# Kernel optimization log

Measured on AMD Instinct MI355X. Metric: run time of the kernel, lower is better.

The kernel has to match this reference:

```python
import jax, jax.numpy as jnp
import numpy as np
import math

Ds = 2048
N = 16384
M = 1024


def setup_inputs() -> dict:
    key = jax.random.key(0)
    kD, kS, kW = jax.random.split(key, 3)
    D = jax.random.normal(kD, (N, Ds), dtype=jnp.float32)
    S = jax.random.normal(kS, (M, Ds), dtype=jnp.float32)
    W = jax.random.normal(kW, (Ds, Ds), dtype=jnp.float32) * 0.01  # init.normal std=0.01
    return {"D": D, "S": S, "W": W}


def reference(D, S, W):
    ds = D.shape[1]
    temperature = 1.0
    # cross-attention: [n, m]
    scores = (D @ S.T) / (math.sqrt(ds) * temperature)
    att_weight = jax.nn.softmax(scores, axis=1)
    att_S = att_weight @ S  # [n, Ds]
    # bilinear per row: logits[i] = D[i] . (W @ att_S[i])  -> fused einsum
    logits = jnp.einsum('nd,de,ne->n', D, W, att_S)
    log_prob = jnp.sum(jax.nn.log_sigmoid(logits))
    return log_prob
```

## Files before the change

### kernel.cpp

```cpp
#include <hip/hip_runtime.h>
#include <stdint.h>

typedef unsigned short u16;
typedef unsigned int u32;
typedef __attribute__((ext_vector_type(8))) short bf16x8;
typedef __attribute__((ext_vector_type(4))) float f32x4;
typedef __attribute__((ext_vector_type(4))) u32 u32x4;

#define DS 2048
#define NROWS 16384
#define MS 1024
#define K2 2048

__device__ __forceinline__ u16 f2bf(float f) {
  u32 u = __float_as_uint(f);
  u32 r = (u + 0x7fffu + ((u >> 16) & 1u)) >> 16;
  return (u16)r;
}

__device__ __forceinline__ void gload16(const u16* g, u16* l) {
  __builtin_amdgcn_global_load_lds(
      (const __attribute__((address_space(1))) void*)g,
      (__attribute__((address_space(3))) void*)l, 16, 0, 0);
}

#define DSR(d, a, IMM) \
  asm volatile("ds_read_b128 %0, %1 offset:%c2" : "=v"(d) : "v"(a), "n"(IMM))
#define CVTPK(d, lo, hi) \
  asm("v_cvt_pk_bf16_f32 %0, %1, %2" : "=v"(d) : "v"(lo), "v"(hi))
#define LGKM(N)                                              \
  asm volatile("s_waitcnt lgkmcnt(" #N ")" ::: "memory");    \
  __builtin_amdgcn_sched_barrier(0)
#define VMW(N) asm volatile("s_waitcnt vmcnt(" #N ")" ::: "memory")
#define SB0() __builtin_amdgcn_sched_barrier(0)
#define PRIO1() __builtin_amdgcn_s_setprio(1)
#define PRIO0() __builtin_amdgcn_s_setprio(0)
#define BAR() __builtin_amdgcn_s_barrier()

#define CVT8(dst, lo, hi)                                         \
  do {                                                            \
    u32 _c0, _c1, _c2, _c3;                                       \
    CVTPK(_c0, lo[0], lo[1]); CVTPK(_c1, lo[2], lo[3]);           \
    CVTPK(_c2, hi[0], hi[1]); CVTPK(_c3, hi[2], hi[3]);           \
    u32x4 _q = {_c0, _c1, _c2, _c3};                              \
    dst = *(bf16x8*)&_q;                                          \
  } while (0)

__global__ __launch_bounds__(256) void k_pre(const float* __restrict__ D,
                                             const float* __restrict__ S,
                                             const float* __restrict__ W,
                                             u16* __restrict__ Dbf,
                                             u16* __restrict__ Bt) {
  __shared__ float lsA[2][64 * 32];
  __shared__ float lsB[2][128 * 32];
  const int bid = blockIdx.x;
  const int tid = threadIdx.x;

  if (bid >= 256) {
    if (bid < 2304) {
      size_t i = (size_t)(bid - 256) * 256 + tid;
#pragma unroll
      for (int it = 0; it < 16; ++it, i += (size_t)2048 * 256) {
        float4 v = ((const float4*)D)[i];
        ushort4 o;
        o.x = f2bf(v.x); o.y = f2bf(v.y); o.z = f2bf(v.z); o.w = f2bf(v.w);
        ((ushort4*)Dbf)[i] = o;
      }
    } else {
      size_t j = (size_t)(bid - 2304) * 256 + tid;
#pragma unroll
      for (int it = 0; it < 16; ++it, j += (size_t)128 * 256) {
        float4 v = ((const float4*)S)[j];
        ushort4 o;
        o.x = f2bf(v.x); o.y = f2bf(v.y); o.z = f2bf(v.z); o.w = f2bf(v.w);
        int m = (int)(j >> 9), c4 = (int)(j & 511);
        ((ushort4*)Bt)[(size_t)m * 1024 + c4] = o;
      }
    }
    return;
  }

  const int wid = tid >> 6, lane = tid & 63;
  const int brow = (bid >> 4) * 64;
  const int bcol = (bid & 15) * 128;
  const int wm = wid >> 1, wn = wid & 1;
  const int l15 = lane & 15, s0 = lane >> 4;

  const int sr = tid >> 3;
  const int soct = (tid & 7) ^ (sr & 7);
  const float* gS = S + (size_t)(brow + sr) * 2048 + soct * 4;
  const float* gW = W + (size_t)(bcol + sr) * 2048 + soct * 4;

  const u32 lbA = (u32)(uintptr_t)&lsA[0][0];
  const u32 lbB = (u32)(uintptr_t)&lsB[0][0];
  const u32 swz = (u32)(((2 * s0) ^ (l15 & 7)) * 16);
  const u32 aA = lbA + (u32)(wm * 32 + l15) * 128 + swz;
  const u32 aAx = aA ^ 16u;
  const u32 aB = lbB + (u32)(wn * 64 + l15) * 128 + swz;
  const u32 aBx = aB ^ 16u;

  f32x4 acc[2][4];
#pragma unroll
  for (int i = 0; i < 2; ++i)
#pragma unroll
    for (int j = 0; j < 4; ++j) acc[i][j] = (f32x4){0.f, 0.f, 0.f, 0.f};

#define VSTG(b, kt)                                                              \
  do {                                                                           \
    gload16((const u16*)(gS + (kt)),             (u16*)(&lsA[b][0] + wid * 256)); \
    gload16((const u16*)(gS + 32 * 2048 + (kt)), (u16*)(&lsA[b][1024] + wid * 256)); \
    gload16((const u16*)(gW + (kt)),             (u16*)(&lsB[b][0] + wid * 256)); \
    gload16((const u16*)(gW + 32 * 2048 + (kt)), (u16*)(&lsB[b][1024] + wid * 256)); \
    gload16((const u16*)(gW + 64 * 2048 + (kt)), (u16*)(&lsB[b][2048] + wid * 256)); \
    gload16((const u16*)(gW + 96 * 2048 + (kt)), (u16*)(&lsB[b][3072] + wid * 256)); \
  } while (0)

  VSTG(0, 0);
#pragma unroll 1
  for (int t = 0; t < 64; ++t) {
    const int b = t & 1;
    const u32 oA = (u32)(b * 8192), oB = (u32)(b * 16384);
    if (t < 63) {
      VSTG(b ^ 1, (t + 1) * 32);
      VMW(6);
    } else {
      VMW(0);
    }
    BAR(); SB0();
    f32x4 qa0, qa1, qa2, qa3;
    f32x4 qb0, qb1, qb2, qb3, qb4, qb5, qb6, qb7;
    DSR(qa0, aA + oA, 0);     DSR(qa1, aAx + oA, 0);
    DSR(qa2, aA + oA, 2048);  DSR(qa3, aAx + oA, 2048);
    DSR(qb0, aB + oB, 0);     DSR(qb1, aBx + oB, 0);
    DSR(qb2, aB + oB, 2048);  DSR(qb3, aBx + oB, 2048);
    DSR(qb4, aB + oB, 4096);  DSR(qb5, aBx + oB, 4096);
    DSR(qb6, aB + oB, 6144);  DSR(qb7, aBx + oB, 6144);
    LGKM(0);
    bf16x8 af[2], bfr[4];
    CVT8(af[0], qa0, qa1); CVT8(af[1], qa2, qa3);
    CVT8(bfr[0], qb0, qb1); CVT8(bfr[1], qb2, qb3);
    CVT8(bfr[2], qb4, qb5); CVT8(bfr[3], qb6, qb7);
    PRIO1();
#pragma unroll
    for (int mi = 0; mi < 2; ++mi)
#pragma unroll
      for (int ni = 0; ni < 4; ++ni)
        acc[mi][ni] = __builtin_amdgcn_mfma_f32_16x16x32_bf16(af[mi], bfr[ni],
                                                              acc[mi][ni], 0, 0, 0);
    PRIO0(); SB0();
    BAR();
  }
#undef VSTG

  const int crow0 = brow + wm * 32 + s0 * 4;
  const int ccol0 = bcol + wn * 64 + l15;
  u16* C = Bt + 2048;
#pragma unroll
  for (int mi = 0; mi < 2; ++mi)
#pragma unroll
    for (int ni = 0; ni < 4; ++ni)
#pragma unroll
      for (int r = 0; r < 4; ++r)
        C[(size_t)(crow0 + mi * 16 + r) * 4096 + (ccol0 + ni * 16)] =
            f2bf(acc[mi][ni][r]);
}

#define SINV 0.022097086912079608f

#define RD_A0(k0, k1, dst)                              \
  DSR(dst[0][0], k0, 0);     DSR(dst[0][1], k1, 0);     \
  DSR(dst[1][0], k0, 2048);  DSR(dst[1][1], k1, 2048);  \
  DSR(dst[2][0], k0, 4096);  DSR(dst[2][1], k1, 4096);  \
  DSR(dst[3][0], k0, 6144);  DSR(dst[3][1], k1, 6144)
#define RD_A1(k0, k1, dst)                              \
  DSR(dst[0][0], k0, 16384); DSR(dst[0][1], k1, 16384); \
  DSR(dst[1][0], k0, 18432); DSR(dst[1][1], k1, 18432); \
  DSR(dst[2][0], k0, 20480); DSR(dst[2][1], k1, 20480); \
  DSR(dst[3][0], k0, 22528); DSR(dst[3][1], k1, 22528)
#define RD_B0(k0, k1, dst)                              \
  DSR(dst[0][0], k0, 0);     DSR(dst[0][1], k1, 0);     \
  DSR(dst[1][0], k0, 2048);  DSR(dst[1][1], k1, 2048)
#define RD_B1(k0, k1, dst)                              \
  DSR(dst[0][0], k0, 16384); DSR(dst[0][1], k1, 16384); \
  DSR(dst[1][0], k0, 18432); DSR(dst[1][1], k1, 18432)

#define MMAQ(AF, BQ, QM, QN)                                                       \
  do {                                                                             \
    _Pragma("unroll") for (int mi = 0; mi < 4; ++mi)                               \
        _Pragma("unroll") for (int ni = 0; ni < 2; ++ni) {                         \
      acc[QM][QN][mi][ni] = __builtin_amdgcn_mfma_f32_16x16x32_bf16(               \
          AF[mi][0], BQ[ni][0], acc[QM][QN][mi][ni], 0, 0, 0);                     \
      acc[QM][QN][mi][ni] = __builtin_amdgcn_mfma_f32_16x16x32_bf16(               \
          AF[mi][1], BQ[ni][1], acc[QM][QN][mi][ni], 0, 0, 0);                     \
    }                                                                              \
  } while (0)

#define STGA(b, h, kt)                                                            \
  do {                                                                            \
    gload16(pA + (size_t)((h) * 128) * K2 + (kt),                                 \
            &lds[(b) * 32768 + (h) * 8192 + wid * 512]);                          \
    gload16(pA + (size_t)((h) * 128 + 64) * K2 + (kt),                            \
            &lds[(b) * 32768 + (h) * 8192 + 4096 + wid * 512]);                   \
  } while (0)
#define STGB(b, h, kt)                                                            \
  do {                                                                            \
    gload16(pB + (size_t)((h) * 128) * K2 + (kt),                                 \
            &lds[(b) * 32768 + 16384 + (h) * 8192 + wid * 512]);                  \
    gload16(pB + (size_t)((h) * 128 + 64) * K2 + (kt),                            \
            &lds[(b) * 32768 + 16384 + (h) * 8192 + 4096 + wid * 512]);           \
  } while (0)

__global__ __launch_bounds__(512, 2) void k_gemm8(const u16* __restrict__ A,
                                                  const u16* __restrict__ Bt,
                                                  float* __restrict__ Pnd) {
  extern __shared__ u16 lds[];
  const int tid = threadIdx.x;
  const int wid = tid >> 6;
  const int lane = tid & 63;
  const int bid = blockIdx.x;
  const int swz = (bid & 7) * 64 + (bid >> 3);
  const int by = swz >> 3, bx = swz & 7;
  const int brow = by * 256, bcol = bx * 256;
  const int wm = wid >> 2, wn = wid & 3;
  const int l15 = lane & 15, s0 = lane >> 4;

  const int tr = tid >> 3;
  const int scol = ((tid & 7) ^ (tr & 7)) << 3;
  const u16* pA = A + (size_t)(brow + tr) * K2 + scol;
  const u16* pB = Bt + (size_t)(bcol + tr) * K2 + scol;

  const u32 lb = (u32)(uintptr_t)(&lds[0]);
  const u32 xorp = ((u32)(s0 ^ (lane & 7))) << 4;
  const u32 aA00 = lb + ((u32)(wm * 64 + l15) << 7) + xorp;
  const u32 aA01 = aA00 ^ 64u;
  const u32 aA10 = aA00 + 65536u;
  const u32 aA11 = aA10 ^ 64u;
  const u32 aB00 = lb + 32768u + ((u32)(wn * 32 + l15) << 7) + xorp;
  const u32 aB01 = aB00 ^ 64u;
  const u32 aB10 = aB00 + 65536u;
  const u32 aB11 = aB10 ^ 64u;

  f32x4 acc[2][2][4][2];
#pragma unroll
  for (int a = 0; a < 2; ++a)
#pragma unroll
    for (int b = 0; b < 2; ++b)
#pragma unroll
      for (int c = 0; c < 4; ++c)
#pragma unroll
        for (int d = 0; d < 2; ++d) acc[a][b][c][d] = (f32x4){0.f, 0.f, 0.f, 0.f};

  bf16x8 afA[4][2], afB[4][2], bq0[2][2], bq1[2][2];

  STGA(0, 0, 0); STGB(0, 0, 0); STGB(0, 1, 0); STGA(0, 1, 0);
  STGA(1, 0, 64);
  VMW(2);
  BAR();
  RD_A0(aA00, aA01, afA);
  RD_B0(aB00, aB01, bq0);

  int kb = 0;
#pragma unroll 1
  for (int j = 0; j < 15; ++j, kb += 128) {
    STGB(1, 0, kb + 64);
    RD_B1(aB00, aB01, bq1);
    LGKM(4); PRIO1(); MMAQ(afA, bq0, 0, 0); PRIO0();
    STGB(1, 1, kb + 64);
    STGA(1, 1, kb + 64);
    RD_A1(aA00, aA01, afB);
    LGKM(8); PRIO1(); MMAQ(afA, bq1, 0, 1); PRIO0(); VMW(4); BAR();
    LGKM(0); PRIO1(); MMAQ(afB, bq0, 1, 0); PRIO0();
    STGA(0, 0, kb + 128);
    STGB(0, 0, kb + 128);
    RD_A0(aA10, aA11, afA);
    RD_B0(aB10, aB11, bq0);
    LGKM(12); PRIO1(); MMAQ(afB, bq1, 1, 1); PRIO0(); VMW(4); BAR();
    STGB(0, 1, kb + 128);
    RD_B1(aB10, aB11, bq1);
    LGKM(4); PRIO1(); MMAQ(afA, bq0, 0, 0); PRIO0();
    STGA(0, 1, kb + 128);
    RD_A1(aA10, aA11, afB);
    LGKM(8); PRIO1(); MMAQ(afA, bq1, 0, 1); PRIO0(); VMW(4); BAR();
    LGKM(0); PRIO1(); MMAQ(afB, bq0, 1, 0); PRIO0();
    STGA(1, 0, kb + 192);
    RD_A0(aA00, aA01, afA);
    RD_B0(aB00, aB01, bq0);
    LGKM(12); PRIO1(); MMAQ(afB, bq1, 1, 1); PRIO0(); VMW(2); BAR();
  }
  {
    STGB(1, 0, kb + 64);
    RD_B1(aB00, aB01, bq1);
    LGKM(4); PRIO1(); MMAQ(afA, bq0, 0, 0); PRIO0();
    STGB(1, 1, kb + 64);
    STGA(1, 1, kb + 64);
    RD_A1(aA00, aA01, afB);
    LGKM(8); PRIO1(); MMAQ(afA, bq1, 0, 1); PRIO0(); VMW(4); BAR();
    LGKM(0); PRIO1(); MMAQ(afB, bq0, 1, 0); PRIO0();
    RD_A0(aA10, aA11, afA);
    RD_B0(aB10, aB11, bq0);
    LGKM(12); PRIO1(); MMAQ(afB, bq1, 1, 1); PRIO0(); VMW(0); BAR();
    RD_B1(aB10, aB11, bq1);
    LGKM(4); PRIO1(); MMAQ(afA, bq0, 0, 0); PRIO0();
    RD_A1(aA10, aA11, afB);
    LGKM(8); PRIO1(); MMAQ(afA, bq1, 0, 1); PRIO0();
    LGKM(0); PRIO1(); MMAQ(afB, bq0, 1, 0); MMAQ(afB, bq1, 1, 1); PRIO0();
  }

  __syncthreads();
  float* red = (float*)&lds[0];

#pragma unroll
  for (int qm = 0; qm < 2; ++qm)
#pragma unroll
    for (int mi = 0; mi < 4; ++mi)
#pragma unroll
      for (int r = 0; r < 4; ++r) {
        float num = 0.f, den = 0.f;
#pragma unroll
        for (int qn = 0; qn < 2; ++qn)
#pragma unroll
          for (int ni = 0; ni < 2; ++ni) {
            float v = acc[qm][qn][mi][ni][r];
            float g = __shfl_xor(v, 1);
            float e = __expf(v * SINV);
            num += e * g;
            den += e;
          }
        num += __shfl_xor(num, 2); den += __shfl_xor(den, 2);
        num += __shfl_xor(num, 4); den += __shfl_xor(den, 4);
        num += __shfl_xor(num, 8); den += __shfl_xor(den, 8);
        if (l15 == 0) {
          int slot = qm * 16 + mi * 4 + r;
          red[((wid * 32 + slot) * 4 + s0) * 2 + 0] = num;
          red[((wid * 32 + slot) * 4 + s0) * 2 + 1] = den;
        }
      }
  __syncthreads();
  {
    int rloc = tid >> 1, which = tid & 1;
    int qm = rloc >> 7, wmr = (rloc >> 6) & 1, mi = (rloc >> 4) & 3;
    int lg = (rloc >> 2) & 3, r = rloc & 3;
    int slot = qm * 16 + mi * 4 + r;
    float v = 0.f;
#pragma unroll
    for (int w2 = 0; w2 < 4; ++w2)
      v += red[(((wmr * 4 + w2) * 32 + slot) * 4 + lg) * 2 + which];
    Pnd[((size_t)(brow + rloc) * 8 + bx) * 2 + which] = v;
  }
}

__global__ __launch_bounds__(256) void k_rowfinal(const float* __restrict__ Pnd,
                                                  float* __restrict__ part) {
  int row = blockIdx.x * 256 + threadIdx.x;
  const float4* p = (const float4*)(Pnd + (size_t)row * 16);
  float num = 0.f, den = 0.f;
#pragma unroll
  for (int i = 0; i < 4; ++i) {
    float4 v = p[i];
    num += v.x + v.z;
    den += v.y + v.w;
  }
  float logit = num / den;
  float ls = (logit >= 0.f) ? -log1pf(__expf(-logit))
                            : (logit - log1pf(__expf(logit)));
  __shared__ float red[4];
#pragma unroll
  for (int off = 32; off > 0; off >>= 1) ls += __shfl_down(ls, off);
  if ((threadIdx.x & 63) == 0) red[threadIdx.x >> 6] = ls;
  __syncthreads();
  if (threadIdx.x == 0) part[blockIdx.x] = red[0] + red[1] + red[2] + red[3];
}

__global__ __launch_bounds__(64) void k_final64(const float* __restrict__ part,
                                                float* __restrict__ out) {
  float v = part[threadIdx.x];
#pragma unroll
  for (int off = 32; off > 0; off >>= 1) v += __shfl_down(v, off);
  if (threadIdx.x == 0) out[0] = v;
}

extern "C" void kernel_launch(void* const* d_in, const int* in_sizes, int n_in,
                              void* d_out, int out_size, void* d_ws, size_t ws_size,
                              hipStream_t stream) {
  const float* D = (const float*)d_in[0];
  const float* S = (const float*)d_in[1];
  const float* W = (const float*)d_in[2];

  char* w = (char*)d_ws;
  u16* Dbf = (u16*)w; w += (size_t)NROWS * DS * 2;
  u16* Bt = (u16*)w;  w += (size_t)DS * DS * 2;
  float* Pnd = (float*)w; w += (size_t)NROWS * 16 * 4;
  float* part = (float*)w;

  (void)hipFuncSetAttribute((const void*)k_gemm8,
                            hipFuncAttributeMaxDynamicSharedMemorySize, 131072);

  k_pre<<<2432, 256, 0, stream>>>(D, S, W, Dbf, Bt);
  k_gemm8<<<512, 512, 131072, stream>>>(Dbf, Bt, Pnd);
  k_rowfinal<<<NROWS / 256, 256, 0, stream>>>(Pnd, part);
  k_final64<<<1, 64, 0, stream>>>(part, (float*)d_out);
}
```

Baseline: 167.1 us.

## Split-K the S·W precompute across two thread groups and reorder main GEMM LDS reads

The prologue kernel now runs 512 threads per block. In the GEMM blocks, two 256-thread groups each handle half of the K dimension with separate LDS buffers, and their partial accumulators are reduced through shared memory before the bf16 store. The conversion blocks process half as many iterations per thread. Separately, the main GEMM loop issues its LDS fragment reads earlier, before the corresponding MFMAs, with adjusted lgkmcnt waits, to hide LDS latency better. The cost is more LDS use and an extra reduction and barrier in the prologue, which lowers occupancy.

```diff
diff --git a/kernel.cpp b/kernel.cpp
--- a/kernel.cpp
+++ b/kernel.cpp
@@ -46,30 +46,29 @@
     dst = *(bf16x8*)&_q;                                          \
   } while (0)
 
-__global__ __launch_bounds__(256) void k_pre(const float* __restrict__ D,
+__global__ __launch_bounds__(512) void k_pre(const float* __restrict__ D,
                                              const float* __restrict__ S,
                                              const float* __restrict__ W,
                                              u16* __restrict__ Dbf,
                                              u16* __restrict__ Bt) {
-  __shared__ float lsA[2][64 * 32];
-  __shared__ float lsB[2][128 * 32];
+  extern __shared__ float ldsf[];
   const int bid = blockIdx.x;
   const int tid = threadIdx.x;
 
   if (bid >= 256) {
     if (bid < 2304) {
-      size_t i = (size_t)(bid - 256) * 256 + tid;
-#pragma unroll
-      for (int it = 0; it < 16; ++it, i += (size_t)2048 * 256) {
+      size_t i = (size_t)(bid - 256) * 512 + tid;
+#pragma unroll
+      for (int it = 0; it < 8; ++it, i += (size_t)2048 * 512) {
         float4 v = ((const float4*)D)[i];
         ushort4 o;
         o.x = f2bf(v.x); o.y = f2bf(v.y); o.z = f2bf(v.z); o.w = f2bf(v.w);
         ((ushort4*)Dbf)[i] = o;
       }
     } else {
-      size_t j = (size_t)(bid - 2304) * 256 + tid;
-#pragma unroll
-      for (int it = 0; it < 16; ++it, j += (size_t)128 * 256) {
+      size_t j = (size_t)(bid - 2304) * 512 + tid;
+#pragma unroll
+      for (int it = 0; it < 8; ++it, j += (size_t)128 * 512) {
         float4 v = ((const float4*)S)[j];
         ushort4 o;
         o.x = f2bf(v.x); o.y = f2bf(v.y); o.z = f2bf(v.z); o.w = f2bf(v.w);
@@ -80,23 +79,26 @@
     return;
   }
 
-  const int wid = tid >> 6, lane = tid & 63;
+  const int g = tid >> 8;
+  const int gtid = tid & 255;
+  const int wid = gtid >> 6, lane = tid & 63;
   const int brow = (bid >> 4) * 64;
   const int bcol = (bid & 15) * 128;
   const int wm = wid >> 1, wn = wid & 1;
   const int l15 = lane & 15, s0 = lane >> 4;
 
-  const int sr = tid >> 3;
-  const int soct = (tid & 7) ^ (sr & 7);
-  const float* gS = S + (size_t)(brow + sr) * 2048 + soct * 4;
-  const float* gW = W + (size_t)(bcol + sr) * 2048 + soct * 4;
-
-  const u32 lbA = (u32)(uintptr_t)&lsA[0][0];
-  const u32 lbB = (u32)(uintptr_t)&lsB[0][0];
+  const int sr = gtid >> 3;
+  const int soct = (gtid & 7) ^ (sr & 7);
+  const float* gS = S + (size_t)(brow + sr) * 2048 + g * 1024 + soct * 4;
+  const float* gW = W + (size_t)(bcol + sr) * 2048 + g * 1024 + soct * 4;
+
+  float* myA = ldsf + g * 12288;
+  float* myB = myA + 4096;
+  const u32 lbg = (u32)(uintptr_t)myA;
   const u32 swz = (u32)(((2 * s0) ^ (l15 & 7)) * 16);
-  const u32 aA = lbA + (u32)(wm * 32 + l15) * 128 + swz;
+  const u32 aA = lbg + (u32)(wm * 32 + l15) * 128 + swz;
   const u32 aAx = aA ^ 16u;
-  const u32 aB = lbB + (u32)(wn * 64 + l15) * 128 + swz;
+  const u32 aB = lbg + 16384u + (u32)(wn * 64 + l15) * 128 + swz;
   const u32 aBx = aB ^ 16u;
 
   f32x4 acc[2][4];
@@ -105,22 +107,22 @@
 #pragma unroll
     for (int j = 0; j < 4; ++j) acc[i][j] = (f32x4){0.f, 0.f, 0.f, 0.f};
 
-#define VSTG(b, kt)                                                              \
-  do {                                                                           \
-    gload16((const u16*)(gS + (kt)),             (u16*)(&lsA[b][0] + wid * 256)); \
-    gload16((const u16*)(gS + 32 * 2048 + (kt)), (u16*)(&lsA[b][1024] + wid * 256)); \
-    gload16((const u16*)(gW + (kt)),             (u16*)(&lsB[b][0] + wid * 256)); \
-    gload16((const u16*)(gW + 32 * 2048 + (kt)), (u16*)(&lsB[b][1024] + wid * 256)); \
-    gload16((const u16*)(gW + 64 * 2048 + (kt)), (u16*)(&lsB[b][2048] + wid * 256)); \
-    gload16((const u16*)(gW + 96 * 2048 + (kt)), (u16*)(&lsB[b][3072] + wid * 256)); \
+#define VSTG(b, kt)                                                               \
+  do {                                                                            \
+    gload16((const u16*)(gS + (kt)),             (u16*)(myA + (b)*2048 + wid*256)); \
+    gload16((const u16*)(gS + 32 * 2048 + (kt)), (u16*)(myA + (b)*2048 + 1024 + wid*256)); \
+    gload16((const u16*)(gW + (kt)),             (u16*)(myB + (b)*4096 + wid*256)); \
+    gload16((const u16*)(gW + 32 * 2048 + (kt)), (u16*)(myB + (b)*4096 + 1024 + wid*256)); \
+    gload16((const u16*)(gW + 64 * 2048 + (kt)), (u16*)(myB + (b)*4096 + 2048 + wid*256)); \
+    gload16((const u16*)(gW + 96 * 2048 + (kt)), (u16*)(myB + (b)*4096 + 3072 + wid*256)); \
   } while (0)
 
   VSTG(0, 0);
 #pragma unroll 1
-  for (int t = 0; t < 64; ++t) {
+  for (int t = 0; t < 32; ++t) {
     const int b = t & 1;
     const u32 oA = (u32)(b * 8192), oB = (u32)(b * 16384);
-    if (t < 63) {
+    if (t < 31) {
       VSTG(b ^ 1, (t + 1) * 32);
       VMW(6);
     } else {
@@ -152,17 +154,31 @@
   }
 #undef VSTG
 
-  const int crow0 = brow + wm * 32 + s0 * 4;
-  const int ccol0 = bcol + wn * 64 + l15;
-  u16* C = Bt + 2048;
-#pragma unroll
-  for (int mi = 0; mi < 2; ++mi)
-#pragma unroll
-    for (int ni = 0; ni < 4; ++ni)
-#pragma unroll
-      for (int r = 0; r < 4; ++r)
-        C[(size_t)(crow0 + mi * 16 + r) * 4096 + (ccol0 + ni * 16)] =
-            f2bf(acc[mi][ni][r]);
+  __syncthreads();
+  float* part = ldsf;
+  if (g == 1) {
+#pragma unroll
+    for (int mi = 0; mi < 2; ++mi)
+#pragma unroll
+      for (int ni = 0; ni < 4; ++ni)
+        *(f32x4*)&part[gtid * 36 + mi * 16 + ni * 4] = acc[mi][ni];
+  }
+  __syncthreads();
+  if (g == 0) {
+    const int crow0 = brow + wm * 32 + s0 * 4;
+    const int ccol0 = bcol + wn * 64 + l15;
+    u16* C = Bt + 2048;
+#pragma unroll
+    for (int mi = 0; mi < 2; ++mi)
+#pragma unroll
+      for (int ni = 0; ni < 4; ++ni) {
+        f32x4 p = *(const f32x4*)&part[gtid * 36 + mi * 16 + ni * 4];
+#pragma unroll
+        for (int r = 0; r < 4; ++r)
+          C[(size_t)(crow0 + mi * 16 + r) * 4096 + (ccol0 + ni * 16)] =
+              f2bf(acc[mi][ni][r] + p[r]);
+      }
+  }
 }
 
 #define SINV 0.022097086912079608f
@@ -262,46 +278,52 @@
   int kb = 0;
 #pragma unroll 1
   for (int j = 0; j < 15; ++j, kb += 128) {
+    RD_B1(aB00, aB01, bq1);
+    RD_A1(aA00, aA01, afB);
+    LGKM(12); PRIO1(); MMAQ(afA, bq0, 0, 0); PRIO0();
     STGB(1, 0, kb + 64);
-    RD_B1(aB00, aB01, bq1);
-    LGKM(4); PRIO1(); MMAQ(afA, bq0, 0, 0); PRIO0();
+    LGKM(8); PRIO1(); MMAQ(afA, bq1, 0, 1); PRIO0();
     STGB(1, 1, kb + 64);
     STGA(1, 1, kb + 64);
-    RD_A1(aA00, aA01, afB);
-    LGKM(8); PRIO1(); MMAQ(afA, bq1, 0, 1); PRIO0(); VMW(4); BAR();
-    LGKM(0); PRIO1(); MMAQ(afB, bq0, 1, 0); PRIO0();
+    VMW(4); BAR();
+    RD_A0(aA10, aA11, afA);
+    LGKM(8); PRIO1(); MMAQ(afB, bq0, 1, 0); PRIO0();
+    RD_B0(aB10, aB11, bq0);
     STGA(0, 0, kb + 128);
     STGB(0, 0, kb + 128);
-    RD_A0(aA10, aA11, afA);
-    RD_B0(aB10, aB11, bq0);
-    LGKM(12); PRIO1(); MMAQ(afB, bq1, 1, 1); PRIO0(); VMW(4); BAR();
+    LGKM(12); PRIO1(); MMAQ(afB, bq1, 1, 1); PRIO0();
+    VMW(4); BAR();
+    RD_B1(aB10, aB11, bq1);
+    RD_A1(aA10, aA11, afB);
+    LGKM(12); PRIO1(); MMAQ(afA, bq0, 0, 0); PRIO0();
     STGB(0, 1, kb + 128);
-    RD_B1(aB10, aB11, bq1);
-    LGKM(4); PRIO1(); MMAQ(afA, bq0, 0, 0); PRIO0();
+    LGKM(8); PRIO1(); MMAQ(afA, bq1, 0, 1); PRIO0();
     STGA(0, 1, kb + 128);
-    RD_A1(aA10, aA11, afB);
-    LGKM(8); PRIO1(); MMAQ(afA, bq1, 0, 1); PRIO0(); VMW(4); BAR();
-    LGKM(0); PRIO1(); MMAQ(afB, bq0, 1, 0); PRIO0();
+    VMW(4); BAR();
+    RD_A0(aA00, aA01, afA);
+    LGKM(8); PRIO1(); MMAQ(afB, bq0, 1, 0); PRIO0();
+    RD_B0(aB00, aB01, bq0);
     STGA(1, 0, kb + 192);
-    RD_A0(aA00, aA01, afA);
-    RD_B0(aB00, aB01, bq0);
-    LGKM(12); PRIO1(); MMAQ(afB, bq1, 1, 1); PRIO0(); VMW(2); BAR();
+    LGKM(12); PRIO1(); MMAQ(afB, bq1, 1, 1); PRIO0();
+    VMW(2); BAR();
   }
   {
+    RD_B1(aB00, aB01, bq1);
+    RD_A1(aA00, aA01, afB);
+    LGKM(12); PRIO1(); MMAQ(afA, bq0, 0, 0); PRIO0();
     STGB(1, 0, kb + 64);
-    RD_B1(aB00, aB01, bq1);
-    LGKM(4); PRIO1(); MMAQ(afA, bq0, 0, 0); PRIO0();
+    LGKM(8); PRIO1(); MMAQ(afA, bq1, 0, 1); PRIO0();
     STGB(1, 1, kb + 64);
     STGA(1, 1, kb + 64);
-    RD_A1(aA00, aA01, afB);
-    LGKM(8); PRIO1(); MMAQ(afA, bq1, 0, 1); PRIO0(); VMW(4); BAR();
-    LGKM(0); PRIO1(); MMAQ(afB, bq0, 1, 0); PRIO0();
+    VMW(4); BAR();
     RD_A0(aA10, aA11, afA);
+    LGKM(8); PRIO1(); MMAQ(afB, bq0, 1, 0); PRIO0();
     RD_B0(aB10, aB11, bq0);
-    LGKM(12); PRIO1(); MMAQ(afB, bq1, 1, 1); PRIO0(); VMW(0); BAR();
+    LGKM(12); PRIO1(); MMAQ(afB, bq1, 1, 1); PRIO0();
+    VMW(0); BAR();
     RD_B1(aB10, aB11, bq1);
-    LGKM(4); PRIO1(); MMAQ(afA, bq0, 0, 0); PRIO0();
     RD_A1(aA10, aA11, afB);
+    LGKM(12); PRIO1(); MMAQ(afA, bq0, 0, 0); PRIO0();
     LGKM(8); PRIO1(); MMAQ(afA, bq1, 0, 1); PRIO0();
     LGKM(0); PRIO1(); MMAQ(afB, bq0, 1, 0); MMAQ(afB, bq1, 1, 1); PRIO0();
   }
@@ -394,8 +416,10 @@
 
   (void)hipFuncSetAttribute((const void*)k_gemm8,
                             hipFuncAttributeMaxDynamicSharedMemorySize, 131072);
-
-  k_pre<<<2432, 256, 0, stream>>>(D, S, W, Dbf, Bt);
+  (void)hipFuncSetAttribute((const void*)k_pre,
+                            hipFuncAttributeMaxDynamicSharedMemorySize, 98304);
+
+  k_pre<<<2432, 512, 98304, stream>>>(D, S, W, Dbf, Bt);
   k_gemm8<<<512, 512, 131072, stream>>>(Dbf, Bt, Pnd);
   k_rowfinal<<<NROWS / 256, 256, 0, stream>>>(Pnd, part);
   k_final64<<<1, 64, 0, stream>>>(part, (float*)d_out);
```

New measurement: 184.1 us. +10.2%, slower.
